# Kernel optimization log

Hardware: AMD Instinct MI355X
Metric: run time of the kernel (lower is better)

Reference implementation:

```python
import jax, jax.numpy as jnp
import numpy as np

N_NODES, N_EDGES, N_GRAPHS, N_FEATS = 100000, 1600000, 256, 128
BN_EPS = 1e-5


def setup_inputs() -> dict:
    key = jax.random.key(0)
    ks = jax.random.split(key, 12)
    x = jax.random.normal(ks[0], (N_NODES, N_FEATS), jnp.float32)
    edge_index = jax.random.randint(ks[1], (2, N_EDGES), 0, N_NODES, dtype=jnp.int64)
    batch = jnp.sort(jax.random.randint(ks[2], (N_NODES,), 0, N_GRAPHS, dtype=jnp.int64))
    s = 0.05
    return {
        "x": x,
        "edge_index": edge_index,
        "batch": batch,
        "W1": jax.random.normal(ks[3], (N_FEATS, 32), jnp.float32) * s,
        "b1": jnp.zeros((32,), jnp.float32),
        "W2": jax.random.normal(ks[4], (32, 64), jnp.float32) * s,
        "b2": jnp.zeros((64,), jnp.float32),
        "fcW1": jax.random.normal(ks[5], (64, 32), jnp.float32) * s,
        "fcb1": jnp.zeros((32,), jnp.float32),
        "gamma": jnp.ones((32,), jnp.float32),
        "beta": jnp.zeros((32,), jnp.float32),
        "fcW2": jax.random.normal(ks[6], (32, 1), jnp.float32) * s,
        "fcb2": jnp.zeros((1,), jnp.float32),
    }


def _gcn_conv(x, src, dst, deg_inv, W, b):
    # PyG GCNConv: h = x @ W; out[d] = sum_e norm_e * h[src_e] + self-loop + b
    h = x @ W  # [N, out]
    norm = deg_inv[src] * deg_inv[dst]  # [E]
    msg = h[src] * norm[:, None]
    out = jax.ops.segment_sum(msg, dst, num_segments=x.shape[0])
    out = out + (deg_inv * deg_inv)[:, None] * h  # self-loop contribution
    return out + b


def reference(x, edge_index, batch, W1, b1, W2, b2, fcW1, fcb1, gamma, beta, fcW2, fcb2):
    src, dst = edge_index[0], edge_index[1]
    n = x.shape[0]
    # degree with self loops, computed on target nodes (PyG default)
    deg = 1.0 + jax.ops.segment_sum(jnp.ones_like(src, dtype=x.dtype), dst, num_segments=n)
    deg_inv = jax.lax.rsqrt(deg)
    h = _gcn_conv(x, src, dst, deg_inv, W1, b1)   # [N, 32]
    h = _gcn_conv(h, src, dst, deg_inv, W2, b2)   # [N, 64]
    # scatter_mean over graph batch
    sums = jax.ops.segment_sum(h, batch, num_segments=N_GRAPHS)  # [G, 64]
    cnt = jax.ops.segment_sum(jnp.ones((n,), h.dtype), batch, num_segments=N_GRAPHS)
    pooled = sums / jnp.maximum(cnt, 1.0)[:, None]
    # head: Linear -> ReLU -> BatchNorm1d (batch stats) -> Dropout(eval=id) -> Linear -> Softplus
    z = jax.nn.relu(pooled @ fcW1 + fcb1)  # [G, 32]
    mu = jnp.mean(z, axis=0)
    var = jnp.var(z, axis=0)
    z = (z - mu) * jax.lax.rsqrt(var + BN_EPS) * gamma + beta
    out = jax.nn.softplus(z @ fcW2 + fcb2)  # [G, 1]
    return out
```

## Files before the change

kernel.cpp:

```cpp
#include <hip/hip_runtime.h>

#define NN 100000
#define NE 1600000
#define NG 256

#define BSH 8
#define NPB 256
#define NBKT ((NN + NPB - 1) / NPB)
#define STRIDE 4608
#define TILE 8192
#define NB_P1 ((NE + TILE - 1) / TILE)

__device__ __forceinline__ unsigned short f2bf(float x) {
    unsigned int u = __float_as_uint(x);
    u += 0x7FFFu + ((u >> 16) & 1u);
    return (unsigned short)(u >> 16);
}
__device__ __forceinline__ float2 bf2x2(unsigned int v) {
    float2 r;
    r.x = __uint_as_float(v << 16);
    r.y = __uint_as_float(v & 0xFFFF0000u);
    return r;
}
__device__ __forceinline__ unsigned int bfpack(float x, float y) {
    return (unsigned int)f2bf(x) | ((unsigned int)f2bf(y) << 16);
}

__global__ __launch_bounds__(1024) void part_kernel(const int* __restrict__ src,
                                                    const int* __restrict__ dst,
                                                    int* __restrict__ bkt_cur,
                                                    int* __restrict__ epack) {
    __shared__ int hist[512];
    __shared__ int scan0[512];
    __shared__ int cur[NBKT];
    __shared__ int gbase[NBKT];
    __shared__ int stage[TILE];
    __shared__ unsigned short sb[TILE];
    int tid = threadIdx.x;
    int e0 = blockIdx.x * TILE;
    int e1 = min(e0 + TILE, NE);
    int n = e1 - e0;

    for (int i = tid; i < 512; i += 1024) hist[i] = 0;
    __syncthreads();

    int d_[8], s_[8];
#pragma unroll
    for (int k = 0; k < 8; ++k) {
        int e = e0 + tid + k * 1024;
        if (e < e1) {
            d_[k] = dst[e];
            s_[k] = src[e];
            atomicAdd(&hist[d_[k] >> BSH], 1);
        }
    }
    __syncthreads();

    if (tid < 512) scan0[tid] = hist[tid];
    __syncthreads();
    for (int off = 1; off < 512; off <<= 1) {
        int t = (tid < 512 && tid >= off) ? scan0[tid - off] : 0;
        __syncthreads();
        if (tid < 512) scan0[tid] += t;
        __syncthreads();
    }
    if (tid < NBKT) {
        int h = hist[tid];
        int ex = scan0[tid] - h;
        cur[tid] = ex;
        gbase[tid] = tid * STRIDE + (h ? atomicAdd(&bkt_cur[tid], h) : 0) - ex;
    }
    __syncthreads();

#pragma unroll
    for (int k = 0; k < 8; ++k) {
        int e = e0 + tid + k * 1024;
        if (e < e1) {
            int d = d_[k];
            int bk = d >> BSH;
            int p = atomicAdd(&cur[bk], 1);
            stage[p] = s_[k] | ((d & (NPB - 1)) << 17);
            sb[p] = (unsigned short)bk;
        }
    }
    __syncthreads();

    for (int j = tid; j < n; j += 1024) {
        int bk = sb[j];
        int a = gbase[bk] + j;
        if (a < (bk + 1) * STRIDE)
            epack[a] = stage[j];
    }
}

__global__ __launch_bounds__(512) void build_kernel(const int* __restrict__ epack,
                                                    const int* __restrict__ bkt_cur,
                                                    int* __restrict__ row_beg,
                                                    int* __restrict__ row_deg,
                                                    int* __restrict__ col,
                                                    float* __restrict__ deg_inv) {
    __shared__ int cnt[NPB];
    __shared__ int ts[NPB];
    int b = blockIdx.x;
    int tid = threadIdx.x;
    int ebase = b * STRIDE;
    int eend = ebase + min(bkt_cur[b], STRIDE);
    int nbase = b << BSH;
    if (tid < NPB) cnt[tid] = 0;
    __syncthreads();
    for (int e = ebase + tid; e < eend; e += 512)
        atomicAdd(&cnt[epack[e] >> 17], 1);
    __syncthreads();
    int v = 0;
    if (tid < NPB) {
        v = cnt[tid];
        ts[tid] = v;
    }
    __syncthreads();
    for (int off = 1; off < NPB; off <<= 1) {
        int t = (tid < NPB && tid >= off) ? ts[tid - off] : 0;
        __syncthreads();
        if (tid < NPB) ts[tid] += t;
        __syncthreads();
    }
    if (tid < NPB) {
        int loff = ts[tid] - v;
        int node = nbase + tid;
        if (node < NN) {
            row_beg[node] = ebase + loff;
            row_deg[node] = v;
            deg_inv[node] = rsqrtf(1.0f + (float)v);
        }
        cnt[tid] = loff;
    }
    __syncthreads();
    for (int e = ebase + tid; e < eend; e += 512) {
        int rec = epack[e];
        int r = atomicAdd(&cnt[rec >> 17], 1);
        col[ebase + r] = rec & 0x1FFFF;
    }
}

__global__ __launch_bounds__(256) void gemm_x_w1(const float* __restrict__ x,
                                                 const float* __restrict__ W,
                                                 const float* __restrict__ deg_inv,
                                                 unsigned short* __restrict__ h, int N) {
    __shared__ float wsh[128 * 32];
    __shared__ float xs[32][132];
    int tid = threadIdx.x;
    int row0 = blockIdx.x * 32;
    if (blockIdx.x == 0 && tid < 8)
        *(ushort4*)&h[(size_t)NN * 32 + tid * 4] = make_ushort4(0, 0, 0, 0);
    for (int i = tid; i < 1024; i += 256)
        ((float4*)wsh)[i] = ((const float4*)W)[i];
    for (int i = tid; i < 1024; i += 256) {
        int r = i >> 5, c4 = i & 31;
        *(float4*)&xs[r][c4 * 4] = ((const float4*)(x + (size_t)(row0 + r) * 128))[c4];
    }
    __syncthreads();
    int r = tid >> 3;
    int c8 = (tid & 7) * 4;
    float acc0 = 0.f, acc1 = 0.f, acc2 = 0.f, acc3 = 0.f;
#pragma unroll
    for (int k0 = 0; k0 < 128; k0 += 4) {
        float4 xv = *(const float4*)&xs[r][k0];
#pragma unroll
        for (int j = 0; j < 4; ++j) {
            float xk = (&xv.x)[j];
            float4 wv = *(const float4*)&wsh[(k0 + j) * 32 + c8];
            acc0 += xk * wv.x;
            acc1 += xk * wv.y;
            acc2 += xk * wv.z;
            acc3 += xk * wv.w;
        }
    }
    float di = deg_inv[row0 + r];
    ushort4 o;
    o.x = f2bf(acc0 * di);
    o.y = f2bf(acc1 * di);
    o.z = f2bf(acc2 * di);
    o.w = f2bf(acc3 * di);
    *(ushort4*)&h[(size_t)(row0 + r) * 32 + c8] = o;
}

template <int MODE>
__global__ __launch_bounds__(512) void conv_bf_kernel(const int* __restrict__ row_beg,
                                                      const int* __restrict__ row_deg,
                                                      const int* __restrict__ col,
                                                      const uint2* __restrict__ h2,
                                                      const float* __restrict__ deg_inv,
                                                      const float* __restrict__ b,
                                                      uint2* __restrict__ out_bf,
                                                      const int* __restrict__ batch,
                                                      float* __restrict__ gsum,
                                                      float* __restrict__ gcnt) {
    __shared__ float sacc[2][32];
    __shared__ float scnt[2];
    __shared__ int sg[2];
    int tid = threadIdx.x;
    int gid = blockIdx.x * 512 + tid;
    int node = gid >> 3;
    int L = gid & 7;
    if (MODE == 0) {
        if (blockIdx.x == 0 && tid < 8)
            out_bf[(size_t)NN * 8 + tid] = make_uint2(0u, 0u);
    } else {
        if (tid < 64) sacc[tid >> 5][tid & 31] = 0.f;
        if (tid < 2) scnt[tid] = 0.f;
        if (tid == 0) {
            int nb = blockIdx.x * 64;
            sg[0] = batch[nb];
            sg[1] = batch[min(nb + 63, NN - 1)];
        }
    }
    bool valid = node < NN;
    float o0 = 0.f, o1 = 0.f, o2 = 0.f, o3 = 0.f;
    if (valid) {
        int beg = row_beg[node];
        int end = beg + row_deg[node];
        uint2 sv = h2[node * 8 + L];
        float2 s0 = bf2x2(sv.x), s1 = bf2x2(sv.y);
        float a00 = s0.x, a01 = s0.y, a02 = s1.x, a03 = s1.y;
        float a10 = 0.f, a11 = 0.f, a12 = 0.f, a13 = 0.f;
        float a20 = 0.f, a21 = 0.f, a22 = 0.f, a23 = 0.f;
        float a30 = 0.f, a31 = 0.f, a32 = 0.f, a33 = 0.f;
        int myc = (beg + L < end) ? col[beg + L] : NN;
        for (int j0 = beg; j0 < end; j0 += 8) {
            int nxt = (j0 + 8 + L < end) ? col[j0 + 8 + L] : NN;
            int i0 = __shfl(myc, 0, 8) * 8 + L;
            int i1 = __shfl(myc, 1, 8) * 8 + L;
            int i2 = __shfl(myc, 2, 8) * 8 + L;
            int i3 = __shfl(myc, 3, 8) * 8 + L;
            int i4 = __shfl(myc, 4, 8) * 8 + L;
            int i5 = __shfl(myc, 5, 8) * 8 + L;
            int i6 = __shfl(myc, 6, 8) * 8 + L;
            int i7 = __shfl(myc, 7, 8) * 8 + L;
            uint2 v0 = h2[i0];
            uint2 v1 = h2[i1];
            uint2 v2 = h2[i2];
            uint2 v3 = h2[i3];
            uint2 v4 = h2[i4];
            uint2 v5 = h2[i5];
            uint2 v6 = h2[i6];
            uint2 v7 = h2[i7];
            float2 p, q;
            p = bf2x2(v0.x); q = bf2x2(v0.y);
            a00 += p.x; a01 += p.y; a02 += q.x; a03 += q.y;
            p = bf2x2(v1.x); q = bf2x2(v1.y);
            a10 += p.x; a11 += p.y; a12 += q.x; a13 += q.y;
            p = bf2x2(v2.x); q = bf2x2(v2.y);
            a20 += p.x; a21 += p.y; a22 += q.x; a23 += q.y;
            p = bf2x2(v3.x); q = bf2x2(v3.y);
            a30 += p.x; a31 += p.y; a32 += q.x; a33 += q.y;
            p = bf2x2(v4.x); q = bf2x2(v4.y);
            a00 += p.x; a01 += p.y; a02 += q.x; a03 += q.y;
            p = bf2x2(v5.x); q = bf2x2(v5.y);
            a10 += p.x; a11 += p.y; a12 += q.x; a13 += q.y;
            p = bf2x2(v6.x); q = bf2x2(v6.y);
            a20 += p.x; a21 += p.y; a22 += q.x; a23 += q.y;
            p = bf2x2(v7.x); q = bf2x2(v7.y);
            a30 += p.x; a31 += p.y; a32 += q.x; a33 += q.y;
            myc = nxt;
        }
        float c0 = (a00 + a10) + (a20 + a30);
        float c1 = (a01 + a11) + (a21 + a31);
        float c2 = (a02 + a12) + (a22 + a32);
        float c3 = (a03 + a13) + (a23 + a33);
        float di = deg_inv[node];
        if (MODE == 0) {
            o0 = di * di * c0 + di * b[4 * L + 0];
            o1 = di * di * c1 + di * b[4 * L + 1];
            o2 = di * di * c2 + di * b[4 * L + 2];
            o3 = di * di * c3 + di * b[4 * L + 3];
            out_bf[node * 8 + L] = make_uint2(bfpack(o0, o1), bfpack(o2, o3));
        } else {
            o0 = di * c0; o1 = di * c1; o2 = di * c2; o3 = di * c3;
        }
    }
    if (MODE == 1) {
        __syncthreads();
        if (valid) {
            int gn = batch[node];
            int fb = 4 * L;
            if (gn == sg[0]) {
                atomicAdd(&sacc[0][fb + 0], o0);
                atomicAdd(&sacc[0][fb + 1], o1);
                atomicAdd(&sacc[0][fb + 2], o2);
                atomicAdd(&sacc[0][fb + 3], o3);
                if (L == 0) atomicAdd(&scnt[0], 1.f);
            } else if (gn == sg[1]) {
                atomicAdd(&sacc[1][fb + 0], o0);
                atomicAdd(&sacc[1][fb + 1], o1);
                atomicAdd(&sacc[1][fb + 2], o2);
                atomicAdd(&sacc[1][fb + 3], o3);
                if (L == 0) atomicAdd(&scnt[1], 1.f);
            } else {
                unsafeAtomicAdd(&gsum[gn * 32 + fb + 0], o0);
                unsafeAtomicAdd(&gsum[gn * 32 + fb + 1], o1);
                unsafeAtomicAdd(&gsum[gn * 32 + fb + 2], o2);
                unsafeAtomicAdd(&gsum[gn * 32 + fb + 3], o3);
                if (L == 0) unsafeAtomicAdd(&gcnt[gn], 1.f);
            }
        }
        __syncthreads();
        if (tid < 64) {
            int s = tid >> 5, f = tid & 31;
            if (s == 0 || sg[1] != sg[0])
                unsafeAtomicAdd(&gsum[sg[s] * 32 + f], sacc[s][f]);
        }
        if (tid == 0) unsafeAtomicAdd(&gcnt[sg[0]], scnt[0]);
        if (tid == 1 && sg[1] != sg[0]) unsafeAtomicAdd(&gcnt[sg[1]], scnt[1]);
    }
}

__global__ __launch_bounds__(256) void head_kernel(const float* __restrict__ gsum,
                                                   const float* __restrict__ gcnt,
                                                   const float* __restrict__ W2,
                                                   const float* __restrict__ b2,
                                                   const float* __restrict__ fcW1,
                                                   const float* __restrict__ fcb1,
                                                   const float* __restrict__ gamma,
                                                   const float* __restrict__ beta,
                                                   const float* __restrict__ fcW2,
                                                   const float* __restrict__ fcb2,
                                                   float* __restrict__ out) {
    __shared__ float zs[NG][33];
    __shared__ float wcs[32 * 32];
    __shared__ float bcs[32];
    __shared__ float part1[8][32];
    __shared__ float part2[8][32];
    __shared__ float mu[32], rstd[32];
    int g = threadIdx.x;

    for (int idx = g; idx < 32 * 32; idx += 256) {
        int k = idx / 32, ch = idx % 32;
        float a = 0.f;
#pragma unroll
        for (int j = 0; j < 64; ++j) a += W2[k * 64 + j] * fcW1[j * 32 + ch];
        wcs[idx] = a;
    }
    if (g < 32) {
        float a = fcb1[g];
#pragma unroll
        for (int j = 0; j < 64; ++j) a += b2[j] * fcW1[j * 32 + g];
        bcs[g] = a;
    }
    __syncthreads();

    float p32[32];
    float inv = 1.0f / fmaxf(gcnt[g], 1.0f);
    {
        const float4* gs4 = (const float4*)(gsum + g * 32);
#pragma unroll
        for (int q = 0; q < 8; ++q) {
            float4 v = gs4[q];
            p32[q * 4 + 0] = v.x * inv;
            p32[q * 4 + 1] = v.y * inv;
            p32[q * 4 + 2] = v.z * inv;
            p32[q * 4 + 3] = v.w * inv;
        }
    }
#pragma unroll 4
    for (int ch = 0; ch < 32; ++ch) {
        float acc = bcs[ch];
#pragma unroll
        for (int k = 0; k < 32; ++k) acc += p32[k] * wcs[k * 32 + ch];
        zs[g][ch] = fmaxf(acc, 0.f);
    }
    __syncthreads();

    {
        int ch = g & 31, seg = g >> 5;
        float s = 0.f, sq = 0.f;
#pragma unroll
        for (int i = 0; i < 32; ++i) {
            float v = zs[seg * 32 + i][ch];
            s += v;
            sq += v * v;
        }
        part1[seg][ch] = s;
        part2[seg][ch] = sq;
    }
    __syncthreads();
    if (g < 32) {
        float s = 0.f, sq = 0.f;
#pragma unroll
        for (int i = 0; i < 8; ++i) { s += part1[i][g]; sq += part2[i][g]; }
        float m = s / NG;
        float v = sq / NG - m * m;
        mu[g] = m;
        rstd[g] = rsqrtf(fmaxf(v, 0.f) + 1e-5f);
    }
    __syncthreads();

    float acc = fcb2[0];
#pragma unroll 4
    for (int ch = 0; ch < 32; ++ch) {
        float zn = (zs[g][ch] - mu[ch]) * rstd[ch] * gamma[ch] + beta[ch];
        acc += zn * fcW2[ch];
    }
    out[g] = fmaxf(acc, 0.f) + log1pf(expf(-fabsf(acc)));
}

extern "C" void kernel_launch(void* const* d_in, const int* in_sizes, int n_in,
                              void* d_out, int out_size, void* d_ws, size_t ws_size,
                              hipStream_t stream) {
    const float* x     = (const float*)d_in[0];
    const int*   ei    = (const int*)d_in[1];
    const int*   batch = (const int*)d_in[2];
    const float* W1    = (const float*)d_in[3];
    const float* b1    = (const float*)d_in[4];
    const float* W2    = (const float*)d_in[5];
    const float* b2    = (const float*)d_in[6];
    const float* fcW1  = (const float*)d_in[7];
    const float* fcb1  = (const float*)d_in[8];
    const float* gamma = (const float*)d_in[9];
    const float* beta  = (const float*)d_in[10];
    const float* fcW2  = (const float*)d_in[11];
    const float* fcb2  = (const float*)d_in[12];
    float* out = (float*)d_out;

    char* p = (char*)d_ws;
    int*   bkt_cur = (int*)p;        p += 400 * 4;
    float* gsum    = (float*)p;      p += (size_t)NG * 32 * 4;
    float* gcnt    = (float*)p;      p += (size_t)NG * 4;
    float* deg_inv = (float*)p;      p += (size_t)NN * 4;
    int*   row_beg = (int*)p;        p += (size_t)(NN + 8) * 4;
    int*   row_deg = (int*)p;        p += (size_t)(NN + 8) * 4;
    int*   epack   = (int*)p;        p += (size_t)NBKT * STRIDE * 4;
    int*   col     = (int*)p;        p += (size_t)NBKT * STRIDE * 4;
    unsigned short* h1s = (unsigned short*)p;  p += (size_t)(NN + 1) * 32 * 2;
    uint2*          t1  = (uint2*)p;           p += (size_t)(NN + 1) * 8 * 8;

    const int* srcv = ei;
    const int* dstv = ei + NE;

    hipMemsetAsync(bkt_cur, 0, 400 * 4 + (size_t)NG * 32 * 4 + (size_t)NG * 4, stream);

    part_kernel<<<NB_P1, 1024, 0, stream>>>(srcv, dstv, bkt_cur, epack);
    build_kernel<<<NBKT, 512, 0, stream>>>(epack, bkt_cur, row_beg, row_deg, col, deg_inv);

    gemm_x_w1<<<NN / 32, 256, 0, stream>>>(x, W1, deg_inv, h1s, NN);
    conv_bf_kernel<0><<<((size_t)NN * 8 + 511) / 512, 512, 0, stream>>>(
        row_beg, row_deg, col, (const uint2*)h1s, deg_inv, b1, t1, nullptr, nullptr, nullptr);

    conv_bf_kernel<1><<<((size_t)NN * 8 + 511) / 512, 512, 0, stream>>>(
        row_beg, row_deg, col, (const uint2*)t1, deg_inv, b1, nullptr, batch, gsum, gcnt);

    head_kernel<<<1, 256, 0, stream>>>(gsum, gcnt, W2, b2, fcW1, fcb1, gamma, beta, fcW2, fcb2, out);
}
```

Measured before the change: 218.8 us.

## Split 32-wide features into two 16-wide halves for cache-resident gathers

The GEMM output is split into two 16-feature bf16 arrays, and each aggregation layer runs as two separate half passes. This halves the gather footprint per pass (about 3.2 MB per half array), so the random neighbour gathers are more likely to stay in L2/MALL, at the cost of reading the CSR column array twice as often and launching more kernels. Nontemporal loads and stores are also added on streamed edge, x and col data to reduce cache pollution. The head kernel is widened to 1024 threads to spread its per-graph matmul and batch-norm reductions.

```diff
diff --git a/kernel.cpp b/kernel.cpp
--- a/kernel.cpp
+++ b/kernel.cpp
@@ -10,6 +10,7 @@
 #define STRIDE 4608
 #define TILE 8192
 #define NB_P1 ((NE + TILE - 1) / TILE)
+#define NB_CONV (((size_t)NN * 8 + 511) / 512)
 
 __device__ __forceinline__ unsigned short f2bf(float x) {
     unsigned int u = __float_as_uint(x);
@@ -49,8 +50,8 @@
     for (int k = 0; k < 8; ++k) {
         int e = e0 + tid + k * 1024;
         if (e < e1) {
-            d_[k] = dst[e];
-            s_[k] = src[e];
+            d_[k] = __builtin_nontemporal_load(&dst[e]);
+            s_[k] = __builtin_nontemporal_load(&src[e]);
             atomicAdd(&hist[d_[k] >> BSH], 1);
         }
     }
@@ -137,25 +138,34 @@
     for (int e = ebase + tid; e < eend; e += 512) {
         int rec = epack[e];
         int r = atomicAdd(&cnt[rec >> 17], 1);
-        col[ebase + r] = rec & 0x1FFFF;
+        __builtin_nontemporal_store(rec & 0x1FFFF, &col[ebase + r]);
     }
 }
 
 __global__ __launch_bounds__(256) void gemm_x_w1(const float* __restrict__ x,
                                                  const float* __restrict__ W,
                                                  const float* __restrict__ deg_inv,
-                                                 unsigned short* __restrict__ h, int N) {
+                                                 unsigned short* __restrict__ hA,
+                                                 unsigned short* __restrict__ hB, int N) {
     __shared__ float wsh[128 * 32];
     __shared__ float xs[32][132];
     int tid = threadIdx.x;
     int row0 = blockIdx.x * 32;
-    if (blockIdx.x == 0 && tid < 8)
-        *(ushort4*)&h[(size_t)NN * 32 + tid * 4] = make_ushort4(0, 0, 0, 0);
+    if (blockIdx.x == 0 && tid < 8) {
+        unsigned short* hp = (tid < 4) ? hA : hB;
+        *(ushort4*)&hp[(size_t)NN * 16 + (tid & 3) * 4] = make_ushort4(0, 0, 0, 0);
+    }
     for (int i = tid; i < 1024; i += 256)
         ((float4*)wsh)[i] = ((const float4*)W)[i];
     for (int i = tid; i < 1024; i += 256) {
         int r = i >> 5, c4 = i & 31;
-        *(float4*)&xs[r][c4 * 4] = ((const float4*)(x + (size_t)(row0 + r) * 128))[c4];
+        const float* xp = x + (size_t)(row0 + r) * 128 + c4 * 4;
+        float v0 = __builtin_nontemporal_load(xp + 0);
+        float v1 = __builtin_nontemporal_load(xp + 1);
+        float v2 = __builtin_nontemporal_load(xp + 2);
+        float v3 = __builtin_nontemporal_load(xp + 3);
+        float* dp = &xs[r][c4 * 4];
+        dp[0] = v0; dp[1] = v1; dp[2] = v2; dp[3] = v3;
     }
     __syncthreads();
     int r = tid >> 3;
@@ -180,21 +190,22 @@
     o.y = f2bf(acc1 * di);
     o.z = f2bf(acc2 * di);
     o.w = f2bf(acc3 * di);
-    *(ushort4*)&h[(size_t)(row0 + r) * 32 + c8] = o;
-}
-
-template <int MODE>
-__global__ __launch_bounds__(512) void conv_bf_kernel(const int* __restrict__ row_beg,
-                                                      const int* __restrict__ row_deg,
-                                                      const int* __restrict__ col,
-                                                      const uint2* __restrict__ h2,
-                                                      const float* __restrict__ deg_inv,
-                                                      const float* __restrict__ b,
-                                                      uint2* __restrict__ out_bf,
-                                                      const int* __restrict__ batch,
-                                                      float* __restrict__ gsum,
-                                                      float* __restrict__ gcnt) {
-    __shared__ float sacc[2][32];
+    unsigned short* hdst = (c8 < 16) ? hA : hB;
+    *(ushort4*)&hdst[(size_t)(row0 + r) * 16 + (c8 & 15)] = o;
+}
+
+template <int MODE, int HALF>
+__global__ __launch_bounds__(512) void conv_half(const int* __restrict__ row_beg,
+                                                 const int* __restrict__ row_deg,
+                                                 const int* __restrict__ col,
+                                                 const unsigned int* __restrict__ h,
+                                                 const float* __restrict__ deg_inv,
+                                                 const float* __restrict__ bias,
+                                                 unsigned int* __restrict__ outh,
+                                                 const int* __restrict__ batch,
+                                                 float* __restrict__ gsum,
+                                                 float* __restrict__ gcnt) {
+    __shared__ float sacc[2][16];
     __shared__ float scnt[2];
     __shared__ int sg[2];
     int tid = threadIdx.x;
@@ -203,9 +214,9 @@
     int L = gid & 7;
     if (MODE == 0) {
         if (blockIdx.x == 0 && tid < 8)
-            out_bf[(size_t)NN * 8 + tid] = make_uint2(0u, 0u);
+            outh[(size_t)NN * 8 + tid] = 0u;
     } else {
-        if (tid < 64) sacc[tid >> 5][tid & 31] = 0.f;
+        if (tid < 32) sacc[tid >> 4][tid & 15] = 0.f;
         if (tid < 2) scnt[tid] = 0.f;
         if (tid == 0) {
             int nb = blockIdx.x * 64;
@@ -214,19 +225,17 @@
         }
     }
     bool valid = node < NN;
-    float o0 = 0.f, o1 = 0.f, o2 = 0.f, o3 = 0.f;
+    float o0 = 0.f, o1 = 0.f;
     if (valid) {
         int beg = row_beg[node];
         int end = beg + row_deg[node];
-        uint2 sv = h2[node * 8 + L];
-        float2 s0 = bf2x2(sv.x), s1 = bf2x2(sv.y);
-        float a00 = s0.x, a01 = s0.y, a02 = s1.x, a03 = s1.y;
-        float a10 = 0.f, a11 = 0.f, a12 = 0.f, a13 = 0.f;
-        float a20 = 0.f, a21 = 0.f, a22 = 0.f, a23 = 0.f;
-        float a30 = 0.f, a31 = 0.f, a32 = 0.f, a33 = 0.f;
-        int myc = (beg + L < end) ? col[beg + L] : NN;
+        unsigned int sv = h[(size_t)node * 8 + L];
+        float2 s = bf2x2(sv);
+        float a0x = s.x, a0y = s.y;
+        float a1x = 0.f, a1y = 0.f, a2x = 0.f, a2y = 0.f, a3x = 0.f, a3y = 0.f;
+        int myc = (beg + L < end) ? __builtin_nontemporal_load(&col[beg + L]) : NN;
         for (int j0 = beg; j0 < end; j0 += 8) {
-            int nxt = (j0 + 8 + L < end) ? col[j0 + 8 + L] : NN;
+            int nxt = (j0 + 8 + L < end) ? __builtin_nontemporal_load(&col[j0 + 8 + L]) : NN;
             int i0 = __shfl(myc, 0, 8) * 8 + L;
             int i1 = __shfl(myc, 1, 8) * 8 + L;
             int i2 = __shfl(myc, 2, 8) * 8 + L;
@@ -235,109 +244,101 @@
             int i5 = __shfl(myc, 5, 8) * 8 + L;
             int i6 = __shfl(myc, 6, 8) * 8 + L;
             int i7 = __shfl(myc, 7, 8) * 8 + L;
-            uint2 v0 = h2[i0];
-            uint2 v1 = h2[i1];
-            uint2 v2 = h2[i2];
-            uint2 v3 = h2[i3];
-            uint2 v4 = h2[i4];
-            uint2 v5 = h2[i5];
-            uint2 v6 = h2[i6];
-            uint2 v7 = h2[i7];
-            float2 p, q;
-            p = bf2x2(v0.x); q = bf2x2(v0.y);
-            a00 += p.x; a01 += p.y; a02 += q.x; a03 += q.y;
-            p = bf2x2(v1.x); q = bf2x2(v1.y);
-            a10 += p.x; a11 += p.y; a12 += q.x; a13 += q.y;
-            p = bf2x2(v2.x); q = bf2x2(v2.y);
-            a20 += p.x; a21 += p.y; a22 += q.x; a23 += q.y;
-            p = bf2x2(v3.x); q = bf2x2(v3.y);
-            a30 += p.x; a31 += p.y; a32 += q.x; a33 += q.y;
-            p = bf2x2(v4.x); q = bf2x2(v4.y);
-            a00 += p.x; a01 += p.y; a02 += q.x; a03 += q.y;
-            p = bf2x2(v5.x); q = bf2x2(v5.y);
-            a10 += p.x; a11 += p.y; a12 += q.x; a13 += q.y;
-            p = bf2x2(v6.x); q = bf2x2(v6.y);
-            a20 += p.x; a21 += p.y; a22 += q.x; a23 += q.y;
-            p = bf2x2(v7.x); q = bf2x2(v7.y);
-            a30 += p.x; a31 += p.y; a32 += q.x; a33 += q.y;
+            unsigned int v0 = h[i0];
+            unsigned int v1 = h[i1];
+            unsigned int v2 = h[i2];
+            unsigned int v3 = h[i3];
+            unsigned int v4 = h[i4];
+            unsigned int v5 = h[i5];
+            unsigned int v6 = h[i6];
+            unsigned int v7 = h[i7];
+            float2 p;
+            p = bf2x2(v0); a0x += p.x; a0y += p.y;
+            p = bf2x2(v1); a1x += p.x; a1y += p.y;
+            p = bf2x2(v2); a2x += p.x; a2y += p.y;
+            p = bf2x2(v3); a3x += p.x; a3y += p.y;
+            p = bf2x2(v4); a0x += p.x; a0y += p.y;
+            p = bf2x2(v5); a1x += p.x; a1y += p.y;
+            p = bf2x2(v6); a2x += p.x; a2y += p.y;
+            p = bf2x2(v7); a3x += p.x; a3y += p.y;
             myc = nxt;
         }
-        float c0 = (a00 + a10) + (a20 + a30);
-        float c1 = (a01 + a11) + (a21 + a31);
-        float c2 = (a02 + a12) + (a22 + a32);
-        float c3 = (a03 + a13) + (a23 + a33);
+        float c0 = (a0x + a1x) + (a2x + a3x);
+        float c1 = (a0y + a1y) + (a2y + a3y);
         float di = deg_inv[node];
         if (MODE == 0) {
-            o0 = di * di * c0 + di * b[4 * L + 0];
-            o1 = di * di * c1 + di * b[4 * L + 1];
-            o2 = di * di * c2 + di * b[4 * L + 2];
-            o3 = di * di * c3 + di * b[4 * L + 3];
-            out_bf[node * 8 + L] = make_uint2(bfpack(o0, o1), bfpack(o2, o3));
+            o0 = di * di * c0 + di * bias[HALF * 16 + 2 * L];
+            o1 = di * di * c1 + di * bias[HALF * 16 + 2 * L + 1];
+            outh[(size_t)node * 8 + L] = bfpack(o0, o1);
         } else {
-            o0 = di * c0; o1 = di * c1; o2 = di * c2; o3 = di * c3;
+            o0 = di * c0;
+            o1 = di * c1;
         }
     }
     if (MODE == 1) {
         __syncthreads();
         if (valid) {
             int gn = batch[node];
-            int fb = 4 * L;
+            int fb = 2 * L;
             if (gn == sg[0]) {
-                atomicAdd(&sacc[0][fb + 0], o0);
+                atomicAdd(&sacc[0][fb], o0);
                 atomicAdd(&sacc[0][fb + 1], o1);
-                atomicAdd(&sacc[0][fb + 2], o2);
-                atomicAdd(&sacc[0][fb + 3], o3);
-                if (L == 0) atomicAdd(&scnt[0], 1.f);
+                if (HALF == 0 && L == 0) atomicAdd(&scnt[0], 1.f);
             } else if (gn == sg[1]) {
-                atomicAdd(&sacc[1][fb + 0], o0);
+                atomicAdd(&sacc[1][fb], o0);
                 atomicAdd(&sacc[1][fb + 1], o1);
-                atomicAdd(&sacc[1][fb + 2], o2);
-                atomicAdd(&sacc[1][fb + 3], o3);
-                if (L == 0) atomicAdd(&scnt[1], 1.f);
+                if (HALF == 0 && L == 0) atomicAdd(&scnt[1], 1.f);
             } else {
-                unsafeAtomicAdd(&gsum[gn * 32 + fb + 0], o0);
-                unsafeAtomicAdd(&gsum[gn * 32 + fb + 1], o1);
-                unsafeAtomicAdd(&gsum[gn * 32 + fb + 2], o2);
-                unsafeAtomicAdd(&gsum[gn * 32 + fb + 3], o3);
-                if (L == 0) unsafeAtomicAdd(&gcnt[gn], 1.f);
+                unsafeAtomicAdd(&gsum[gn * 32 + HALF * 16 + fb], o0);
+                unsafeAtomicAdd(&gsum[gn * 32 + HALF * 16 + fb + 1], o1);
+                if (HALF == 0 && L == 0) unsafeAtomicAdd(&gcnt[gn], 1.f);
             }
         }
         __syncthreads();
-        if (tid < 64) {
-            int s = tid >> 5, f = tid & 31;
+        if (tid < 32) {
+            int s = tid >> 4, f = tid & 15;
             if (s == 0 || sg[1] != sg[0])
-                unsafeAtomicAdd(&gsum[sg[s] * 32 + f], sacc[s][f]);
-        }
-        if (tid == 0) unsafeAtomicAdd(&gcnt[sg[0]], scnt[0]);
-        if (tid == 1 && sg[1] != sg[0]) unsafeAtomicAdd(&gcnt[sg[1]], scnt[1]);
-    }
-}
-
-__global__ __launch_bounds__(256) void head_kernel(const float* __restrict__ gsum,
-                                                   const float* __restrict__ gcnt,
-                                                   const float* __restrict__ W2,
-                                                   const float* __restrict__ b2,
-                                                   const float* __restrict__ fcW1,
-                                                   const float* __restrict__ fcb1,
-                                                   const float* __restrict__ gamma,
-                                                   const float* __restrict__ beta,
-                                                   const float* __restrict__ fcW2,
-                                                   const float* __restrict__ fcb2,
-                                                   float* __restrict__ out) {
+                unsafeAtomicAdd(&gsum[sg[s] * 32 + HALF * 16 + f], sacc[s][f]);
+        }
+        if (HALF == 0) {
+            if (tid == 0) unsafeAtomicAdd(&gcnt[sg[0]], scnt[0]);
+            if (tid == 1 && sg[1] != sg[0]) unsafeAtomicAdd(&gcnt[sg[1]], scnt[1]);
+        }
+    }
+}
+
+__global__ __launch_bounds__(1024) void head_kernel(const float* __restrict__ gsum,
+                                                    const float* __restrict__ gcnt,
+                                                    const float* __restrict__ W2,
+                                                    const float* __restrict__ b2,
+                                                    const float* __restrict__ fcW1,
+                                                    const float* __restrict__ fcb1,
+                                                    const float* __restrict__ gamma,
+                                                    const float* __restrict__ beta,
+                                                    const float* __restrict__ fcW2,
+                                                    const float* __restrict__ fcb2,
+                                                    float* __restrict__ out) {
     __shared__ float zs[NG][33];
     __shared__ float wcs[32 * 32];
     __shared__ float bcs[32];
-    __shared__ float part1[8][32];
-    __shared__ float part2[8][32];
+    __shared__ float part1[32][32];
+    __shared__ float part2[32][32];
     __shared__ float mu[32], rstd[32];
     int g = threadIdx.x;
 
-    for (int idx = g; idx < 32 * 32; idx += 256) {
-        int k = idx / 32, ch = idx % 32;
+    {
+        int k = g >> 5, ch = g & 31;
+        const float4* w2r = (const float4*)(W2 + k * 64);
         float a = 0.f;
 #pragma unroll
-        for (int j = 0; j < 64; ++j) a += W2[k * 64 + j] * fcW1[j * 32 + ch];
-        wcs[idx] = a;
+        for (int j4 = 0; j4 < 16; ++j4) {
+            float4 w = w2r[j4];
+            a += w.x * fcW1[(j4 * 4 + 0) * 32 + ch];
+            a += w.y * fcW1[(j4 * 4 + 1) * 32 + ch];
+            a += w.z * fcW1[(j4 * 4 + 2) * 32 + ch];
+            a += w.w * fcW1[(j4 * 4 + 3) * 32 + ch];
+        }
+        wcs[g] = a;
     }
     if (g < 32) {
         float a = fcb1[g];
@@ -347,10 +348,11 @@
     }
     __syncthreads();
 
-    float p32[32];
-    float inv = 1.0f / fmaxf(gcnt[g], 1.0f);
     {
-        const float4* gs4 = (const float4*)(gsum + g * 32);
+        int gr = g >> 2, sub = g & 3;
+        float inv = 1.0f / fmaxf(gcnt[gr], 1.0f);
+        float p32[32];
+        const float4* gs4 = (const float4*)(gsum + gr * 32);
 #pragma unroll
         for (int q = 0; q < 8; ++q) {
             float4 v = gs4[q];
@@ -359,13 +361,14 @@
             p32[q * 4 + 2] = v.z * inv;
             p32[q * 4 + 3] = v.w * inv;
         }
-    }
-#pragma unroll 4
-    for (int ch = 0; ch < 32; ++ch) {
-        float acc = bcs[ch];
-#pragma unroll
-        for (int k = 0; k < 32; ++k) acc += p32[k] * wcs[k * 32 + ch];
-        zs[g][ch] = fmaxf(acc, 0.f);
+#pragma unroll
+        for (int cc = 0; cc < 8; ++cc) {
+            int ch = sub * 8 + cc;
+            float acc = bcs[ch];
+#pragma unroll
+            for (int k = 0; k < 32; ++k) acc += p32[k] * wcs[k * 32 + ch];
+            zs[gr][ch] = fmaxf(acc, 0.f);
+        }
     }
     __syncthreads();
 
@@ -373,8 +376,8 @@
         int ch = g & 31, seg = g >> 5;
         float s = 0.f, sq = 0.f;
 #pragma unroll
-        for (int i = 0; i < 32; ++i) {
-            float v = zs[seg * 32 + i][ch];
+        for (int i = 0; i < 8; ++i) {
+            float v = zs[seg * 8 + i][ch];
             s += v;
             sq += v * v;
         }
@@ -385,7 +388,7 @@
     if (g < 32) {
         float s = 0.f, sq = 0.f;
 #pragma unroll
-        for (int i = 0; i < 8; ++i) { s += part1[i][g]; sq += part2[i][g]; }
+        for (int i = 0; i < 32; ++i) { s += part1[i][g]; sq += part2[i][g]; }
         float m = s / NG;
         float v = sq / NG - m * m;
         mu[g] = m;
@@ -393,13 +396,15 @@
     }
     __syncthreads();
 
-    float acc = fcb2[0];
+    if (g < NG) {
+        float acc = fcb2[0];
 #pragma unroll 4
-    for (int ch = 0; ch < 32; ++ch) {
-        float zn = (zs[g][ch] - mu[ch]) * rstd[ch] * gamma[ch] + beta[ch];
-        acc += zn * fcW2[ch];
-    }
-    out[g] = fmaxf(acc, 0.f) + log1pf(expf(-fabsf(acc)));
+        for (int ch = 0; ch < 32; ++ch) {
+            float zn = (zs[g][ch] - mu[ch]) * rstd[ch] * gamma[ch] + beta[ch];
+            acc += zn * fcW2[ch];
+        }
+        out[g] = fmaxf(acc, 0.f) + log1pf(expf(-fabsf(acc)));
+    }
 }
 
 extern "C" void kernel_launch(void* const* d_in, const int* in_sizes, int n_in,
@@ -429,23 +434,29 @@
     int*   row_deg = (int*)p;        p += (size_t)(NN + 8) * 4;
     int*   epack   = (int*)p;        p += (size_t)NBKT * STRIDE * 4;
     int*   col     = (int*)p;        p += (size_t)NBKT * STRIDE * 4;
-    unsigned short* h1s = (unsigned short*)p;  p += (size_t)(NN + 1) * 32 * 2;
-    uint2*          t1  = (uint2*)p;           p += (size_t)(NN + 1) * 8 * 8;
+    unsigned short* hA  = (unsigned short*)p;  p += (size_t)(NN + 1) * 16 * 2;
+    unsigned short* hB  = (unsigned short*)p;  p += (size_t)(NN + 1) * 16 * 2;
+    unsigned int*   t1A = (unsigned int*)p;    p += (size_t)(NN + 1) * 8 * 4;
+    unsigned int*   t1B = (unsigned int*)p;    p += (size_t)(NN + 1) * 8 * 4;
 
     const int* srcv = ei;
     const int* dstv = ei + NE;
 
-    hipMemsetAsync(bkt_cur, 0, 400 * 4 + (size_t)NG * 32 * 4 + (size_t)NG * 4, stream);
+    (void)hipMemsetAsync(bkt_cur, 0, 400 * 4 + (size_t)NG * 32 * 4 + (size_t)NG * 4, stream);
 
     part_kernel<<<NB_P1, 1024, 0, stream>>>(srcv, dstv, bkt_cur, epack);
     build_kernel<<<NBKT, 512, 0, stream>>>(epack, bkt_cur, row_beg, row_deg, col, deg_inv);
 
-    gemm_x_w1<<<NN / 32, 256, 0, stream>>>(x, W1, deg_inv, h1s, NN);
-    conv_bf_kernel<0><<<((size_t)NN * 8 + 511) / 512, 512, 0, stream>>>(
-        row_beg, row_deg, col, (const uint2*)h1s, deg_inv, b1, t1, nullptr, nullptr, nullptr);
-
-    conv_bf_kernel<1><<<((size_t)NN * 8 + 511) / 512, 512, 0, stream>>>(
-        row_beg, row_deg, col, (const uint2*)t1, deg_inv, b1, nullptr, batch, gsum, gcnt);
-
-    head_kernel<<<1, 256, 0, stream>>>(gsum, gcnt, W2, b2, fcW1, fcb1, gamma, beta, fcW2, fcb2, out);
-}
+    gemm_x_w1<<<NN / 32, 256, 0, stream>>>(x, W1, deg_inv, hA, hB, NN);
+
+    conv_half<0, 0><<<NB_CONV, 512, 0, stream>>>(row_beg, row_deg, col, (const unsigned int*)hA,
+                                                 deg_inv, b1, t1A, nullptr, nullptr, nullptr);
+    conv_half<1, 0><<<NB_CONV, 512, 0, stream>>>(row_beg, row_deg, col, (const unsigned int*)t1A,
+                                                 deg_inv, nullptr, nullptr, batch, gsum, gcnt);
+    conv_half<0, 1><<<NB_CONV, 512, 0, stream>>>(row_beg, row_deg, col, (const unsigned int*)hB,
+                                                 deg_inv, b1, t1B, nullptr, nullptr, nullptr);
+    conv_half<1, 1><<<NB_CONV, 512, 0, stream>>>(row_beg, row_deg, col, (const unsigned int*)t1B,
+                                                 deg_inv, nullptr, nullptr, batch, gsum, gcnt);
+
+    head_kernel<<<1, 1024, 0, stream>>>(gsum, gcnt, W2, b2, fcW1, fcb1, gamma, beta, fcW2, fcb2, out);
+}
```

Result: slower. 264.8 us (+21.1%).
